# Optimization experiments

Hardware: AMD Instinct MI355X
Metric: run time of the kernel (lower is better)

Reference implementation:

```python
import jax, jax.numpy as jnp
import numpy as np
import math
from functools import lru_cache

DIM = 64   # num_inputs
HID = 32   # hidden_dim
B = 1024
LOG2 = math.log(2.0)
LOG_2PI = math.log(2.0 * math.pi)


@lru_cache(maxsize=None)
def _masks(out_f, in_f, dim):
    ob, ib = out_f // dim, in_f // dim
    md = np.zeros((out_f, in_f), np.float32)
    mo = np.ones((out_f, in_f), np.float32)
    for i in range(dim):
        md[i * ob:(i + 1) * ob, i * ib:(i + 1) * ib] = 1.0
        mo[i * ob:(i + 1) * ob, i * ib:] = 0.0
    return jnp.asarray(md), jnp.asarray(mo)


def masked_weight(x, grad, W, dw, b, dim):
    # W: (out_f, in_f), dw: (out_f, 1), b: (out_f,)
    out_f, in_f = W.shape
    ob, ib = out_f // dim, in_f // dim
    md, mo = _masks(out_f, in_f, dim)
    w = jnp.exp(W) * md + W * mo                      # positive diag blocks, masked lower blocks
    wsn = jnp.sum(w * w, axis=-1, keepdims=True)      # (out_f, 1) weight-norm denom^2
    wn = jnp.exp(dw) * w / jnp.sqrt(wsn)              # weight-normalized matrix
    wpl = dw + W - 0.5 * jnp.log(wsn)                 # log of diag-block entries, (out_f, in_f)
    # extract diagonal blocks: (dim, ob, dim, ib) -> diag over block index -> (ob, ib, dim)
    blocks = jnp.diagonal(wpl.reshape(dim, ob, dim, ib), axis1=0, axis2=2)
    g = jnp.transpose(blocks, (2, 0, 1))              # (dim, ob, ib) == torch g per-sample
    out = x @ wn.T + b
    if grad is None:
        return out, jnp.broadcast_to(g[None], (x.shape[0],) + g.shape)
    # grad: (Bt, dim, a, c); log-domain block 'matmul' via logsumexp over shared axis a(=ib)
    comb = g[None, :, :, None, :] + jnp.swapaxes(grad, -1, -2)[:, :, None, :, :]  # (Bt,dim,ob,c,ib)
    return out, jax.nn.logsumexp(comb, axis=-1)       # (Bt, dim, ob, c)


def tanh_layer(x, grad):
    g = -2.0 * (x - LOG2 + jax.nn.softplus(-2.0 * x))
    return jnp.tanh(x), g.reshape(grad.shape) + grad


def bnaf_flow(x, p0, p1, p2, gate, dim):
    out, grad = masked_weight(x, None, *p0, dim)
    out, grad = tanh_layer(out, grad)
    out, grad = masked_weight(out, grad, *p1, dim)
    out, grad = tanh_layer(out, grad)
    out, grad = masked_weight(out, grad, *p2, dim)
    g = grad.reshape(grad.shape[0], dim)              # squeeze (B, dim, 1, 1) -> (B, dim)
    if gate is None:
        return out, jnp.sum(g, -1)
    s = jax.nn.sigmoid(gate)
    out = s * out + (1.0 - s) * x
    ldj = jnp.sum(jax.nn.softplus(g + gate) - jax.nn.softplus(gate), -1)
    return out, ldj


def _forward(x, params, gates):
    ldj = 0.0
    for f in range(3):
        gate = gates[f] if f < 2 else None
        x, l = bnaf_flow(x, params[f][0], params[f][1], params[f][2], gate, DIM)
        ldj = ldj + l
        if f < 2:
            x = x[:, ::-1]                            # Permutation('flip'), log-det 0
    log_p_y = jnp.sum(-0.5 * x * x - 0.5 * LOG_2PI, -1)
    return log_p_y + ldj                              # (B,)


def setup_inputs() -> dict:
    key = jax.random.key(0)
    ks = iter(jax.random.split(key, 64))
    d, dh = DIM, DIM * HID
    shapes = [(dh, d), (dh, dh), (d, dh)]
    inp = {"x": jax.random.normal(next(ks), (B, d), jnp.float32)}
    for f in range(3):
        for l, (o, i) in enumerate(shapes):
            inp[f"W{f}_{l}"] = 0.1 * jax.random.normal(next(ks), (o, i), jnp.float32)
            inp[f"dw{f}_{l}"] = jnp.log(jax.random.uniform(next(ks), (o, 1), jnp.float32, 0.1, 1.0))
            inp[f"b{f}_{l}"] = 0.01 * jax.random.normal(next(ks), (o,), jnp.float32)
    inp["gate0"] = jax.random.normal(next(ks), (1,), jnp.float32)
    inp["gate1"] = jax.random.normal(next(ks), (1,), jnp.float32)
    return inp


def reference(x, W0_0, dw0_0, b0_0, W0_1, dw0_1, b0_1, W0_2, dw0_2, b0_2,
              W1_0, dw1_0, b1_0, W1_1, dw1_1, b1_1, W1_2, dw1_2, b1_2,
              W2_0, dw2_0, b2_0, W2_1, dw2_1, b2_1, W2_2, dw2_2, b2_2,
              gate0, gate1):
    params = [
        [(W0_0, dw0_0, b0_0), (W0_1, dw0_1, b0_1), (W0_2, dw0_2, b0_2)],
        [(W1_0, dw1_0, b1_0), (W1_1, dw1_1, b1_1), (W1_2, dw1_2, b1_2)],
        [(W2_0, dw2_0, b2_0), (W2_1, dw2_1, b2_1), (W2_2, dw2_2, b2_2)],
    ]
    return _forward(x, params, (gate0, gate1))
```

## Files before the change

### kernel.cpp

```cpp
#include <hip/hip_runtime.h>
#include <hip/hip_bf16.h>
#include <math.h>


#define DIMN 64
#define BATCH 1024
#define HIDF 2048
#define SPLITK 4
#define NT2 32

typedef __attribute__((ext_vector_type(8))) short short8;
typedef __attribute__((ext_vector_type(4))) float floatx4;

__device__ __forceinline__ float softplusf_(float t) {
    return fmaxf(t, 0.f) + log1pf(__expf(-fabsf(t)));
}

__device__ __forceinline__ float bf2f(short v) {
    union { unsigned u; float f; } x;
    x.u = ((unsigned)(unsigned short)v) << 16;
    return x.f;
}

__device__ __forceinline__ void gl_lds16(const void* g, void* l) {
    __builtin_amdgcn_global_load_lds(
        (const __attribute__((address_space(1))) unsigned int*)g,
        (__attribute__((address_space(3))) unsigned int*)l, 16, 0, 0);
}

__device__ __forceinline__ void tanh_sech2_(float p, float& th, float& s2) {
    float t = __expf(-2.f * fabsf(p));
    float opt = 1.f + t;
    float inv = 1.f / opt;
    th = copysignf((1.f - t) * inv, p);
    s2 = 4.f * t * inv * inv;
}

template<int INF>
__device__ __forceinline__ void prep_row(
    const float* __restrict__ W, const float* __restrict__ dw,
    void* __restrict__ wn_out, float* __restrict__ eg,
    int r, int lane, int out_f, int ob, int ib, int transpose, int bf16out)
{
    constexpr int NI = INF / 64;
    int d = r / ob;
    int c0 = d * ib;
    int c1 = c0 + ib;
    const float* Wr = W + (size_t)r * INF;

    float vv[NI];
    float ss = 0.f;
#pragma unroll
    for (int i = 0; i < NI; ++i) {
        int c = lane + i * 64;
        float wraw = Wr[c];
        float wv = (c < c0) ? wraw : ((c < c1) ? __expf(wraw) : 0.f);
        vv[i] = wv;
        ss += wv * wv;
    }
    for (int off = 32; off > 0; off >>= 1) ss += __shfl_xor(ss, off, 64);

    float dwr = dw[r];
    float scale = __expf(dwr) / sqrtf(ss);
    float logt = dwr - 0.5f * __logf(ss);

#pragma unroll
    for (int i = 0; i < NI; ++i) {
        int c = lane + i * 64;
        float val = scale * vv[i];
        if (bf16out) {
            ((__hip_bfloat16*)wn_out)[(size_t)r * INF + c] = __float2bfloat16(val);
        } else if (transpose) {
            ((float*)wn_out)[(size_t)c * out_f + r] = val;
        } else {
            ((float*)wn_out)[(size_t)r * INF + c] = val;
        }
    }
    if (lane < ib) eg[(size_t)r * ib + lane] = __expf(logt + Wr[c0 + lane]);
}

struct PrepIn { const float *W0, *dw0, *W1, *dw1, *W2, *dw2; };

__global__ __launch_bounds__(64) void prep_mega(
    PrepIn p0, PrepIn p1, PrepIn p2,
    float* __restrict__ wn0T_all, float* __restrict__ eg0_all,
    __hip_bfloat16* __restrict__ wn1_all, float* __restrict__ e1_all,
    __hip_bfloat16* __restrict__ wn2b_all, float* __restrict__ e2_all)
{
    int blk = blockIdx.x;
    int lane = threadIdx.x;
    int f = blk / 4160;
    int rem = blk - f * 4160;
    PrepIn P = (f == 0) ? p0 : ((f == 1) ? p1 : p2);

    float* wn0T = wn0T_all + (size_t)f * DIMN * HIDF;
    float* eg0  = eg0_all  + (size_t)f * HIDF;
    __hip_bfloat16* wn1 = wn1_all + (size_t)f * HIDF * HIDF;
    float* e1   = e1_all   + (size_t)f * HIDF * 32;
    __hip_bfloat16* wn2b = wn2b_all + (size_t)f * DIMN * HIDF;
    float* e2   = e2_all   + (size_t)f * DIMN * 32;

    if (rem < HIDF) {
        prep_row<DIMN>(P.W0, P.dw0, wn0T, eg0, rem, lane, HIDF, 32, 1, 1, 0);
    } else if (rem < 2 * HIDF) {
        prep_row<HIDF>(P.W1, P.dw1, wn1, e1, rem - HIDF, lane, HIDF, 32, 32, 0, 1);
    } else {
        prep_row<HIDF>(P.W2, P.dw2, wn2b, e2, rem - 2 * HIDF, lane, DIMN, 1, 32, 0, 1);
    }
}

__global__ __launch_bounds__(256) void gemm0_act(
    const float* __restrict__ xin, const float* __restrict__ wn0T,
    const float* __restrict__ bias, const float* __restrict__ eg0,
    __hip_bfloat16* __restrict__ h0, __hip_bfloat16* __restrict__ g0e)
{
    __shared__ float xs[16][DIMN];
    int b0 = blockIdx.y * 16;
    {
        const float4* src = (const float4*)(xin + (size_t)b0 * DIMN);
        ((float4*)xs)[threadIdx.x] = src[threadIdx.x];
    }
    __syncthreads();
    int n = blockIdx.x * 256 + threadIdx.x;

    float acc[16];
#pragma unroll
    for (int j = 0; j < 16; ++j) acc[j] = 0.f;

#pragma unroll 4
    for (int c4 = 0; c4 < 16; ++c4) {
        int c = c4 * 4;
        float w0 = wn0T[(size_t)(c + 0) * HIDF + n];
        float w1 = wn0T[(size_t)(c + 1) * HIDF + n];
        float w2 = wn0T[(size_t)(c + 2) * HIDF + n];
        float w3 = wn0T[(size_t)(c + 3) * HIDF + n];
#pragma unroll
        for (int j = 0; j < 16; ++j) {
            float4 x4 = *(const float4*)&xs[j][c];
            acc[j] = fmaf(x4.x, w0, acc[j]);
            acc[j] = fmaf(x4.y, w1, acc[j]);
            acc[j] = fmaf(x4.z, w2, acc[j]);
            acc[j] = fmaf(x4.w, w3, acc[j]);
        }
    }
    float bv = bias[n], egv = eg0[n];
#pragma unroll
    for (int j = 0; j < 16; ++j) {
        float p = acc[j] + bv;
        float th, s2;
        tanh_sech2_(p, th, s2);
        size_t idx = (size_t)(b0 + j) * HIDF + n;
        h0[idx] = __float2bfloat16(th);
        g0e[idx] = __float2bfloat16(egv * s2);
    }
}

#define G1BK 64
__global__ __launch_bounds__(256) void gemm1_part(
    const __hip_bfloat16* __restrict__ A, const __hip_bfloat16* __restrict__ B,
    __hip_bfloat16* __restrict__ part)
{
    __shared__ short As[128 * 64];
    __shared__ short Bs[128 * 64];
    const int K = HIDF, N = HIDF;
    int tid = threadIdx.x;
    int lane = tid & 63;
    int wave = tid >> 6;
    int n0 = blockIdx.x * 128;
    int m0 = blockIdx.y * 128;
    int kbase = blockIdx.z * (K / SPLITK);
    int wr = wave >> 1;
    int wc = wave & 1;

    int rf = lane & 15;
    int q = lane >> 4;

    const char* agp[4];
    const char* bgp[4];
    char* alds[4];
    char* blds[4];
#pragma unroll
    for (int s = 0; s < 4; ++s) {
        int c = tid + s * 256;
        int row = c >> 3;
        int kc = (c & 7) ^ (row & 7);
        agp[s] = (const char*)A + ((size_t)(m0 + row) * K + kbase) * 2 + kc * 16;
        bgp[s] = (const char*)B + ((size_t)(n0 + row) * K + kbase) * 2 + kc * 16;
        alds[s] = (char*)As + c * 16;
        blds[s] = (char*)Bs + c * 16;
    }

    floatx4 acc[4][4];
#pragma unroll
    for (int i = 0; i < 4; ++i)
#pragma unroll
        for (int j = 0; j < 4; ++j) acc[i][j] = (floatx4){0.f, 0.f, 0.f, 0.f};

    int rowA0 = wr * 64 + rf;
    int rowB0 = wc * 64 + rf;

    for (int k0 = 0; k0 < K / SPLITK; k0 += G1BK) {
        size_t kb = (size_t)k0 * 2;
        __syncthreads();
#pragma unroll
        for (int s = 0; s < 4; ++s) {
            gl_lds16(agp[s] + kb, alds[s]);
            gl_lds16(bgp[s] + kb, blds[s]);
        }
        __syncthreads();

#pragma unroll
        for (int s = 0; s < 2; ++s) {
            short8 af[4], bfv[4];
#pragma unroll
            for (int i = 0; i < 4; ++i) {
                int row = rowA0 + i * 16;
                af[i] = *(const short8*)&As[row * 64 + (((s * 4 + q) ^ (row & 7)) * 8)];
            }
#pragma unroll
            for (int j = 0; j < 4; ++j) {
                int row = rowB0 + j * 16;
                bfv[j] = *(const short8*)&Bs[row * 64 + (((s * 4 + q) ^ (row & 7)) * 8)];
            }
#pragma unroll
            for (int i = 0; i < 4; ++i)
#pragma unroll
                for (int j = 0; j < 4; ++j)
                    acc[i][j] = __builtin_amdgcn_mfma_f32_16x16x32_bf16(af[i], bfv[j], acc[i][j], 0, 0, 0);
        }
    }

    __hip_bfloat16* pk = part + (size_t)blockIdx.z * BATCH * HIDF;
    int col = lane & 15;
    int rq = (lane >> 4) * 4;
#pragma unroll
    for (int i = 0; i < 4; ++i) {
#pragma unroll
        for (int j = 0; j < 4; ++j) {
            int n = n0 + wc * 64 + j * 16 + col;
#pragma unroll
            for (int r = 0; r < 4; ++r) {
                int m = m0 + wr * 64 + i * 16 + rq + r;
                pk[(size_t)m * N + n] = __float2bfloat16(acc[i][j][r]);
            }
        }
    }
}

__global__ __launch_bounds__(256) void act_grad_gemm2(
    const __hip_bfloat16* __restrict__ part, const float* __restrict__ bias,
    const float* __restrict__ e1, const __hip_bfloat16* __restrict__ g0e,
    const __hip_bfloat16* __restrict__ wn2b,
    __hip_bfloat16* __restrict__ grad1e, float* __restrict__ out2p)
{
    __shared__ char smem[17408 + 8704 + 8192];
    float* g0s = (float*)smem;
    short* h1s = (short*)(smem + 17408);
    short* Bs2 = (short*)(smem + 17408 + 8704);

    int tid = threadIdx.x;
    int lane = tid & 63;
    int wave = tid >> 6;
    int n0 = blockIdx.x * 64;
    int b0 = blockIdx.y * 64;

    {
        int c0c = tid, c1c = tid + 256;
        int r0 = c0c >> 3, k0c = (c0c & 7) ^ (r0 & 7);
        int r1 = c1c >> 3, k1c = (c1c & 7) ^ (r1 & 7);
        gl_lds16((const char*)wn2b + ((size_t)r0 * HIDF + n0) * 2 + k0c * 16,
                 (char*)Bs2 + c0c * 16);
        gl_lds16((const char*)wn2b + ((size_t)r1 * HIDF + n0) * 2 + k1c * 16,
                 (char*)Bs2 + c1c * 16);
    }

    for (int s = tid; s < 512; s += 256) {
        int row = s >> 3, c8 = s & 7;
        short8 v = *(const short8*)((const short*)g0e +
                                    (size_t)(b0 + row) * HIDF + n0 + c8 * 8);
        float4 lo = { bf2f(v[0]), bf2f(v[1]), bf2f(v[2]), bf2f(v[3]) };
        float4 hi = { bf2f(v[4]), bf2f(v[5]), bf2f(v[6]), bf2f(v[7]) };
        *(float4*)&g0s[row * 68 + c8 * 8] = lo;
        *(float4*)&g0s[row * 68 + c8 * 8 + 4] = hi;
    }

    int g = tid >> 6;
    int nl = tid & 63;
    int n = n0 + nl;

    float4 er[8];
    const float4* e1r = (const float4*)(e1 + (size_t)n * 32);
#pragma unroll
    for (int qq = 0; qq < 8; ++qq) er[qq] = e1r[qq];

    float bv = bias[n];
    int kb2 = nl & 32;

    __syncthreads();

#pragma unroll
    for (int t = 0; t < 16; ++t) {
        int bl = g * 16 + t;
        int b = b0 + bl;
        size_t idx = (size_t)b * HIDF + n;
        float pre = bv;
#pragma unroll
        for (int p = 0; p < SPLITK; ++p)
            pre += __bfloat162float(part[(size_t)p * BATCH * HIDF + idx]);
        float th, s2;
        tanh_sech2_(pre, th, s2);
        const float* g0row = &g0s[bl * 68 + kb2];
        float dot = 0.f;
#pragma unroll
        for (int qq = 0; qq < 8; ++qq) {
            float4 gv = *(const float4*)&g0row[qq * 4];
            dot = fmaf(gv.x, er[qq].x, dot);
            dot = fmaf(gv.y, er[qq].y, dot);
            dot = fmaf(gv.z, er[qq].z, dot);
            dot = fmaf(gv.w, er[qq].w, dot);
        }
        __hip_bfloat16 thb = __float2bfloat16(th);
        h1s[bl * 68 + nl] = *(const short*)&thb;
        grad1e[idx] = __float2bfloat16(dot * s2);
    }
    __syncthreads();

    int rf = lane & 15;
    int q = lane >> 4;
    floatx4 acc2[4];
#pragma unroll
    for (int j = 0; j < 4; ++j) acc2[j] = (floatx4){0.f, 0.f, 0.f, 0.f};

#pragma unroll
    for (int s = 0; s < 2; ++s) {
        int rowa = wave * 16 + rf;
        short8 af = *(const short8*)&h1s[rowa * 68 + s * 32 + q * 8];
#pragma unroll
        for (int j = 0; j < 4; ++j) {
            int rowb = j * 16 + rf;
            int cp = (s * 4 + q) ^ (rowb & 7);
            short8 bfv = *(const short8*)&Bs2[rowb * 64 + cp * 8];
            acc2[j] = __builtin_amdgcn_mfma_f32_16x16x32_bf16(af, bfv, acc2[j], 0, 0, 0);
        }
    }

    float* outk = out2p + (size_t)blockIdx.x * BATCH * DIMN;
    int col = lane & 15;
    int rq = (lane >> 4) * 4;
#pragma unroll
    for (int j = 0; j < 4; ++j) {
#pragma unroll
        for (int r = 0; r < 4; ++r) {
            int m = b0 + wave * 16 + rq + r;
            outk[(size_t)m * DIMN + j * 16 + col] = acc2[j][r];
        }
    }
}

__global__ __launch_bounds__(256) void tail_trans(
    const float* __restrict__ out2p, const float* __restrict__ b2,
    const float* __restrict__ e2, const __hip_bfloat16* __restrict__ grad1e,
    const float* __restrict__ x_cur, const float* __restrict__ gate,
    float* __restrict__ x_next, float* __restrict__ ldj, int accum_ldj)
{
    int tid = threadIdx.x;
    int b = blockIdx.x * 4 + (tid >> 6);
    int n = tid & 63;

    float o = b2[n];
#pragma unroll
    for (int p = 0; p < NT2; ++p)
        o += out2p[(size_t)p * BATCH * DIMN + (size_t)b * DIMN + n];

    float gt = gate[0];
    float sg = 1.f / (1.f + __expf(-gt));
    float xo = sg * o + (1.f - sg) * x_cur[(size_t)b * DIMN + n];
    x_next[(size_t)b * DIMN + (63 - n)] = xo;

    const short8* gr = (const short8*)((const short*)grad1e + (size_t)b * HIDF + n * 32);
    const float4* gc = (const float4*)(e2 + n * 32);
    float s = 0.f;
#pragma unroll
    for (int q = 0; q < 4; ++q) {
        short8 a8 = gr[q];
        float4 c0 = gc[2 * q], c1 = gc[2 * q + 1];
        s = fmaf(bf2f(a8[0]), c0.x, s);
        s = fmaf(bf2f(a8[1]), c0.y, s);
        s = fmaf(bf2f(a8[2]), c0.z, s);
        s = fmaf(bf2f(a8[3]), c0.w, s);
        s = fmaf(bf2f(a8[4]), c1.x, s);
        s = fmaf(bf2f(a8[5]), c1.y, s);
        s = fmaf(bf2f(a8[6]), c1.z, s);
        s = fmaf(bf2f(a8[7]), c1.w, s);
    }
    float gF = __logf(fmaxf(s, 1e-45f));
    float contrib = softplusf_(gF + gt) - softplusf_(gt);
    for (int off = 32; off > 0; off >>= 1) contrib += __shfl_xor(contrib, off, 64);
    if (n == 0) ldj[b] = accum_ldj ? (ldj[b] + contrib) : contrib;
}

__global__ __launch_bounds__(256) void tail_final(
    const float* __restrict__ out2p, const float* __restrict__ b2,
    const float* __restrict__ e2, const __hip_bfloat16* __restrict__ grad1e,
    const float* __restrict__ ldj, float* __restrict__ out)
{
    int tid = threadIdx.x;
    int b = blockIdx.x * 4 + (tid >> 6);
    int n = tid & 63;

    float o = b2[n];
#pragma unroll
    for (int p = 0; p < NT2; ++p)
        o += out2p[(size_t)p * BATCH * DIMN + (size_t)b * DIMN + n];

    const short8* gr = (const short8*)((const short*)grad1e + (size_t)b * HIDF + n * 32);
    const float4* gc = (const float4*)(e2 + n * 32);
    float s = 0.f;
#pragma unroll
    for (int q = 0; q < 4; ++q) {
        short8 a8 = gr[q];
        float4 c0 = gc[2 * q], c1 = gc[2 * q + 1];
        s = fmaf(bf2f(a8[0]), c0.x, s);
        s = fmaf(bf2f(a8[1]), c0.y, s);
        s = fmaf(bf2f(a8[2]), c0.z, s);
        s = fmaf(bf2f(a8[3]), c0.w, s);
        s = fmaf(bf2f(a8[4]), c1.x, s);
        s = fmaf(bf2f(a8[5]), c1.y, s);
        s = fmaf(bf2f(a8[6]), c1.z, s);
        s = fmaf(bf2f(a8[7]), c1.w, s);
    }
    float gF = __logf(fmaxf(s, 1e-45f));

    float contrib = gF - 0.5f * o * o - 0.91893853320467274f;
    for (int off = 32; off > 0; off >>= 1) contrib += __shfl_xor(contrib, off, 64);
    if (n == 0) out[b] = ldj[b] + contrib;
}

extern "C" void kernel_launch(void* const* d_in, const int* in_sizes, int n_in,
                              void* d_out, int out_size, void* d_ws, size_t ws_size,
                              hipStream_t stream)
{
    (void)in_sizes; (void)n_in; (void)out_size; (void)ws_size;

    const float* x = (const float*)d_in[0];
    const float* gates[2] = { (const float*)d_in[28], (const float*)d_in[29] };

    char* ws = (char*)d_ws;
    size_t ofs = 0;
    auto alloc = [&](size_t bytes) { char* p = ws + ofs; ofs += (bytes + 255) & ~(size_t)255; return p; };

    __hip_bfloat16* wn1_all  = (__hip_bfloat16*)alloc((size_t)3 * HIDF * HIDF * 2);
    __hip_bfloat16* wn2b_all = (__hip_bfloat16*)alloc((size_t)3 * DIMN * HIDF * 2);
    float* wn0T_all = (float*)alloc((size_t)3 * DIMN * HIDF * 4);
    float* eg0_all  = (float*)alloc((size_t)3 * HIDF * 4);
    float* e1_all   = (float*)alloc((size_t)3 * HIDF * 32 * 4);
    float* e2_all   = (float*)alloc((size_t)3 * DIMN * 32 * 4);
    __hip_bfloat16* h0   = (__hip_bfloat16*)alloc((size_t)BATCH * HIDF * 2);
    __hip_bfloat16* part = (__hip_bfloat16*)alloc((size_t)SPLITK * BATCH * HIDF * 2);
    __hip_bfloat16* g0e    = (__hip_bfloat16*)alloc((size_t)BATCH * HIDF * 2);
    __hip_bfloat16* grad1e = (__hip_bfloat16*)alloc((size_t)BATCH * HIDF * 2);
    float* out2p  = (float*)alloc((size_t)NT2 * BATCH * DIMN * 4);
    float* x1     = (float*)alloc((size_t)BATCH * DIMN * 4);
    float* x2     = (float*)alloc((size_t)BATCH * DIMN * 4);
    float* ldj    = (float*)alloc(BATCH * 4);
    float* outp   = (float*)d_out;

    auto W = [&](int f, int i) { return (const float*)d_in[1 + f * 9 + i]; };

    PrepIn p0 = { W(0,0), W(0,1), W(0,3), W(0,4), W(0,6), W(0,7) };
    PrepIn p1 = { W(1,0), W(1,1), W(1,3), W(1,4), W(1,6), W(1,7) };
    PrepIn p2 = { W(2,0), W(2,1), W(2,3), W(2,4), W(2,6), W(2,7) };

    prep_mega<<<dim3(3 * 4160), dim3(64), 0, stream>>>(
        p0, p1, p2, wn0T_all, eg0_all, wn1_all, e1_all, wn2b_all, e2_all);

    gemm0_act<<<dim3(8, BATCH / 16), dim3(256), 0, stream>>>(
        x, wn0T_all, W(0,2), eg0_all, h0, g0e);

    const float* xcur = x;
    float* xnexts[2] = { x1, x2 };

    for (int f = 0; f < 3; ++f) {
        size_t fo1 = (size_t)f * HIDF * HIDF;
        size_t fo2 = (size_t)f * DIMN * HIDF;

        gemm1_part<<<dim3(HIDF / 128, BATCH / 128, SPLITK), dim3(256), 0, stream>>>(
            h0, wn1_all + fo1, part);

        act_grad_gemm2<<<dim3(HIDF / 64, BATCH / 64), dim3(256), 0, stream>>>(
            part, W(f,5), e1_all + (size_t)f * HIDF * 32, g0e,
            wn2b_all + fo2, grad1e, out2p);

        if (f < 2) {
            tail_trans<<<dim3(BATCH / 4), dim3(256), 0, stream>>>(
                out2p, W(f,8), e2_all + (size_t)f * DIMN * 32, grad1e,
                xcur, gates[f], xnexts[f], ldj, f);

            gemm0_act<<<dim3(8, BATCH / 16), dim3(256), 0, stream>>>(
                xnexts[f], wn0T_all + (size_t)(f + 1) * DIMN * HIDF, W(f + 1, 2),
                eg0_all + (size_t)(f + 1) * HIDF, h0, g0e);

            xcur = xnexts[f];
        } else {
            tail_final<<<dim3(BATCH / 4), dim3(256), 0, stream>>>(
                out2p, W(2,8), e2_all + (size_t)2 * DIMN * 32, grad1e, ldj, outp);
        }
    }
}
```

Before: 291.4 us.

## Exploit block-triangular weight structure to skip zero blocks across all kernels

The masked weights are block lower-triangular, so every kernel now limits its work to the nonzero region. The prep kernel packs four rows per block and loads and writes only the nonzero columns. gemm0 shortens its K loop per block, and gemm1 returns early or truncates the K range for split-K partitions that lie above the diagonal. The act/gemm2 and tail kernels read and accumulate only the partitions and MFMA tiles that can be nonzero. Unwritten zero regions of the weight buffers and skipped partial sums are assumed to be zero or never read, which relies on the indexing being exactly consistent across kernels.

```diff
diff --git a/kernel.cpp b/kernel.cpp
--- a/kernel.cpp
+++ b/kernel.cpp
@@ -10,6 +10,7 @@
 #define NT2 32
 
 typedef __attribute__((ext_vector_type(8))) short short8;
+typedef __attribute__((ext_vector_type(4))) short short4v;
 typedef __attribute__((ext_vector_type(4))) float floatx4;
 
 __device__ __forceinline__ float softplusf_(float t) {
@@ -36,61 +37,78 @@
     s2 = 4.f * t * inv * inv;
 }
 
-template<int INF>
-__device__ __forceinline__ void prep_row(
+
+__device__ __forceinline__ void prep_row0(
     const float* __restrict__ W, const float* __restrict__ dw,
-    void* __restrict__ wn_out, float* __restrict__ eg,
-    int r, int lane, int out_f, int ob, int ib, int transpose, int bf16out)
-{
-    constexpr int NI = INF / 64;
-    int d = r / ob;
-    int c0 = d * ib;
-    int c1 = c0 + ib;
-    const float* Wr = W + (size_t)r * INF;
-
-    float vv[NI];
+    float* __restrict__ wn0T, float* __restrict__ eg0, int r, int lane)
+{
+    int d = r >> 5;
+    const float* Wr = W + (size_t)r * 64;
+    float wraw = Wr[lane];
+    float wv = (lane < d) ? wraw : ((lane == d) ? __expf(wraw) : 0.f);
+    float ss = wv * wv;
+    for (int off = 32; off > 0; off >>= 1) ss += __shfl_xor(ss, off, 64);
+    float dwr = dw[r];
+    float scale = __expf(dwr) / sqrtf(ss);
+    wn0T[(size_t)lane * HIDF + r] = scale * wv;
+    if (lane == 0) eg0[r] = __expf(dwr - 0.5f * __logf(ss) + Wr[d]);
+}
+
+__device__ __forceinline__ void prep_row_wide(
+    const float* __restrict__ W, const float* __restrict__ dw,
+    __hip_bfloat16* __restrict__ wn, float* __restrict__ eg,
+    int r, int lane, int d, int ni, int nw)
+{
+    int c0 = d * 32, c1 = c0 + 32;
+    const float* Wr = W + (size_t)r * 2048;
+    float4 vv[8];
     float ss = 0.f;
 #pragma unroll
-    for (int i = 0; i < NI; ++i) {
-        int c = lane + i * 64;
-        float wraw = Wr[c];
-        float wv = (c < c0) ? wraw : ((c < c1) ? __expf(wraw) : 0.f);
-        vv[i] = wv;
-        ss += wv * wv;
+    for (int i = 0; i < 8; ++i) {
+        vv[i] = (float4){0.f, 0.f, 0.f, 0.f};
+        if (i < ni) {
+            int cb = i * 256 + lane * 4;
+            float4 v = *(const float4*)&Wr[cb];
+            float w0 = (cb + 0 < c0) ? v.x : ((cb + 0 < c1) ? __expf(v.x) : 0.f);
+            float w1 = (cb + 1 < c0) ? v.y : ((cb + 1 < c1) ? __expf(v.y) : 0.f);
+            float w2 = (cb + 2 < c0) ? v.z : ((cb + 2 < c1) ? __expf(v.z) : 0.f);
+            float w3 = (cb + 3 < c0) ? v.w : ((cb + 3 < c1) ? __expf(v.w) : 0.f);
+            vv[i] = (float4){w0, w1, w2, w3};
+            ss += w0 * w0 + w1 * w1 + w2 * w2 + w3 * w3;
+        }
     }
     for (int off = 32; off > 0; off >>= 1) ss += __shfl_xor(ss, off, 64);
-
     float dwr = dw[r];
     float scale = __expf(dwr) / sqrtf(ss);
     float logt = dwr - 0.5f * __logf(ss);
-
-#pragma unroll
-    for (int i = 0; i < NI; ++i) {
-        int c = lane + i * 64;
-        float val = scale * vv[i];
-        if (bf16out) {
-            ((__hip_bfloat16*)wn_out)[(size_t)r * INF + c] = __float2bfloat16(val);
-        } else if (transpose) {
-            ((float*)wn_out)[(size_t)c * out_f + r] = val;
-        } else {
-            ((float*)wn_out)[(size_t)r * INF + c] = val;
-        }
-    }
-    if (lane < ib) eg[(size_t)r * ib + lane] = __expf(logt + Wr[c0 + lane]);
+#pragma unroll
+    for (int i = 0; i < 8; ++i) {
+        if (i < nw) {
+            int cb = i * 256 + lane * 4;
+            __hip_bfloat16 b0 = __float2bfloat16(scale * vv[i].x);
+            __hip_bfloat16 b1 = __float2bfloat16(scale * vv[i].y);
+            __hip_bfloat16 b2 = __float2bfloat16(scale * vv[i].z);
+            __hip_bfloat16 b3 = __float2bfloat16(scale * vv[i].w);
+            short4v pk = { *(short*)&b0, *(short*)&b1, *(short*)&b2, *(short*)&b3 };
+            *(short4v*)((short*)wn + (size_t)r * 2048 + cb) = pk;
+        }
+    }
+    if (lane < 32) eg[(size_t)r * 32 + lane] = __expf(logt + Wr[c0 + lane]);
 }
 
 struct PrepIn { const float *W0, *dw0, *W1, *dw1, *W2, *dw2; };
 
-__global__ __launch_bounds__(64) void prep_mega(
+__global__ __launch_bounds__(256) void prep_mega(
     PrepIn p0, PrepIn p1, PrepIn p2,
     float* __restrict__ wn0T_all, float* __restrict__ eg0_all,
     __hip_bfloat16* __restrict__ wn1_all, float* __restrict__ e1_all,
     __hip_bfloat16* __restrict__ wn2b_all, float* __restrict__ e2_all)
 {
     int blk = blockIdx.x;
-    int lane = threadIdx.x;
-    int f = blk / 4160;
-    int rem = blk - f * 4160;
+    int wave = threadIdx.x >> 6;
+    int lane = threadIdx.x & 63;
+    int f = blk / 1040;
+    int rem = blk - f * 1040;
     PrepIn P = (f == 0) ? p0 : ((f == 1) ? p1 : p2);
 
     float* wn0T = wn0T_all + (size_t)f * DIMN * HIDF;
@@ -100,12 +118,15 @@
     __hip_bfloat16* wn2b = wn2b_all + (size_t)f * DIMN * HIDF;
     float* e2   = e2_all   + (size_t)f * DIMN * 32;
 
-    if (rem < HIDF) {
-        prep_row<DIMN>(P.W0, P.dw0, wn0T, eg0, rem, lane, HIDF, 32, 1, 1, 0);
-    } else if (rem < 2 * HIDF) {
-        prep_row<HIDF>(P.W1, P.dw1, wn1, e1, rem - HIDF, lane, HIDF, 32, 32, 0, 1);
+    if (rem < 512) {
+        int r = rem * 4 + wave;
+        prep_row0(P.W0, P.dw0, wn0T, eg0, r, lane);
+    } else if (rem < 1024) {
+        int r = (rem - 512) * 4 + wave;
+        prep_row_wide(P.W1, P.dw1, wn1, e1, r, lane, r >> 5, (r >> 8) + 1, (r >> 8) + 1);
     } else {
-        prep_row<HIDF>(P.W2, P.dw2, wn2b, e2, rem - 2 * HIDF, lane, DIMN, 1, 32, 0, 1);
+        int r = (rem - 1024) * 4 + wave;
+        prep_row_wide(P.W2, P.dw2, wn2b, e2, r, lane, r, (r >> 3) + 1, 8);
     }
 }
 
@@ -127,8 +148,9 @@
 #pragma unroll
     for (int j = 0; j < 16; ++j) acc[j] = 0.f;
 
-#pragma unroll 4
-    for (int c4 = 0; c4 < 16; ++c4) {
+    int c4max = 2 * blockIdx.x + 2;
+#pragma unroll 2
+    for (int c4 = 0; c4 < c4max; ++c4) {
         int c = c4 * 4;
         float w0 = wn0T[(size_t)(c + 0) * HIDF + n];
         float w1 = wn0T[(size_t)(c + 1) * HIDF + n];
@@ -160,15 +182,20 @@
     const __hip_bfloat16* __restrict__ A, const __hip_bfloat16* __restrict__ B,
     __hip_bfloat16* __restrict__ part)
 {
+    const int K = HIDF, N = HIDF;
+    int jn = blockIdx.x;
+    int kbase = blockIdx.z * (K / SPLITK);
+    int kend = (jn + 1) * 128 - kbase;
+    if (kend <= 0) return;
+    if (kend > K / SPLITK) kend = K / SPLITK;
+
     __shared__ short As[128 * 64];
     __shared__ short Bs[128 * 64];
-    const int K = HIDF, N = HIDF;
     int tid = threadIdx.x;
     int lane = tid & 63;
     int wave = tid >> 6;
-    int n0 = blockIdx.x * 128;
+    int n0 = jn * 128;
     int m0 = blockIdx.y * 128;
-    int kbase = blockIdx.z * (K / SPLITK);
     int wr = wave >> 1;
     int wc = wave & 1;
 
@@ -199,7 +226,7 @@
     int rowA0 = wr * 64 + rf;
     int rowB0 = wc * 64 + rf;
 
-    for (int k0 = 0; k0 < K / SPLITK; k0 += G1BK) {
+    for (int k0 = 0; k0 < kend; k0 += G1BK) {
         size_t kb = (size_t)k0 * 2;
         __syncthreads();
 #pragma unroll
@@ -261,8 +288,11 @@
     int tid = threadIdx.x;
     int lane = tid & 63;
     int wave = tid >> 6;
-    int n0 = blockIdx.x * 64;
+    int bx = blockIdx.x;
+    int n0 = bx * 64;
     int b0 = blockIdx.y * 64;
+    int np = (bx >> 3) + 1;
+    int jact0 = bx >> 3;
 
     {
         int c0c = tid, c1c = tid + 256;
@@ -295,6 +325,10 @@
 
     float bv = bias[n];
     int kb2 = nl & 32;
+    const __hip_bfloat16* pp0 = part;
+    const __hip_bfloat16* pp1 = part + (size_t)1 * BATCH * HIDF;
+    const __hip_bfloat16* pp2 = part + (size_t)2 * BATCH * HIDF;
+    const __hip_bfloat16* pp3 = part + (size_t)3 * BATCH * HIDF;
 
     __syncthreads();
 
@@ -303,10 +337,10 @@
         int bl = g * 16 + t;
         int b = b0 + bl;
         size_t idx = (size_t)b * HIDF + n;
-        float pre = bv;
-#pragma unroll
-        for (int p = 0; p < SPLITK; ++p)
-            pre += __bfloat162float(part[(size_t)p * BATCH * HIDF + idx]);
+        float pre = bv + __bfloat162float(pp0[idx]);
+        if (np > 1) pre += __bfloat162float(pp1[idx]);
+        if (np > 2) pre += __bfloat162float(pp2[idx]);
+        if (np > 3) pre += __bfloat162float(pp3[idx]);
         float th, s2;
         tanh_sech2_(pre, th, s2);
         const float* g0row = &g0s[bl * 68 + kb2];
@@ -337,22 +371,26 @@
         short8 af = *(const short8*)&h1s[rowa * 68 + s * 32 + q * 8];
 #pragma unroll
         for (int j = 0; j < 4; ++j) {
-            int rowb = j * 16 + rf;
-            int cp = (s * 4 + q) ^ (rowb & 7);
-            short8 bfv = *(const short8*)&Bs2[rowb * 64 + cp * 8];
-            acc2[j] = __builtin_amdgcn_mfma_f32_16x16x32_bf16(af, bfv, acc2[j], 0, 0, 0);
-        }
-    }
-
-    float* outk = out2p + (size_t)blockIdx.x * BATCH * DIMN;
+            if (j >= jact0) {
+                int rowb = j * 16 + rf;
+                int cp = (s * 4 + q) ^ (rowb & 7);
+                short8 bfv = *(const short8*)&Bs2[rowb * 64 + cp * 8];
+                acc2[j] = __builtin_amdgcn_mfma_f32_16x16x32_bf16(af, bfv, acc2[j], 0, 0, 0);
+            }
+        }
+    }
+
+    float* outk = out2p + (size_t)bx * BATCH * DIMN;
     int col = lane & 15;
     int rq = (lane >> 4) * 4;
 #pragma unroll
     for (int j = 0; j < 4; ++j) {
-#pragma unroll
-        for (int r = 0; r < 4; ++r) {
-            int m = b0 + wave * 16 + rq + r;
-            outk[(size_t)m * DIMN + j * 16 + col] = acc2[j][r];
+        if (j >= jact0) {
+#pragma unroll
+            for (int r = 0; r < 4; ++r) {
+                int m = b0 + wave * 16 + rq + r;
+                outk[(size_t)m * DIMN + j * 16 + col] = acc2[j][r];
+            }
         }
     }
 }
@@ -368,8 +406,8 @@
     int n = tid & 63;
 
     float o = b2[n];
-#pragma unroll
-    for (int p = 0; p < NT2; ++p)
+    int pmax = n >> 1;
+    for (int p = 0; p <= pmax; ++p)
         o += out2p[(size_t)p * BATCH * DIMN + (size_t)b * DIMN + n];
 
     float gt = gate[0];
@@ -409,8 +447,8 @@
     int n = tid & 63;
 
     float o = b2[n];
-#pragma unroll
-    for (int p = 0; p < NT2; ++p)
+    int pmax = n >> 1;
+    for (int p = 0; p <= pmax; ++p)
         o += out2p[(size_t)p * BATCH * DIMN + (size_t)b * DIMN + n];
 
     const short8* gr = (const short8*)((const short*)grad1e + (size_t)b * HIDF + n * 32);
@@ -471,7 +509,7 @@
     PrepIn p1 = { W(1,0), W(1,1), W(1,3), W(1,4), W(1,6), W(1,7) };
     PrepIn p2 = { W(2,0), W(2,1), W(2,3), W(2,4), W(2,6), W(2,7) };
 
-    prep_mega<<<dim3(3 * 4160), dim3(64), 0, stream>>>(
+    prep_mega<<<dim3(3 * 1040), dim3(256), 0, stream>>>(
         p0, p1, p2, wn0T_all, eg0_all, wn1_all, e1_all, wn2b_all, e2_all);
 
     gemm0_act<<<dim3(8, BATCH / 16), dim3(256), 0, stream>>>(
```

Result: slower. 343.3 us (+17.8%).

## Exploit block-triangular weight mask to skip zero tiles in hidden GEMMs

Applied to the files above, without the earlier changes.

The hidden-layer GEMM now launches only the (n-tile, k-split) pairs that can hold nonzero weights under the autoregressive block-lower-triangular mask, using constant lookup tables to map blocks to tiles and truncate the K loop. The following activation kernel sums only the split-K partials that were actually written for each column range and skips MFMAs on zero weight blocks in the output projection. This removes roughly half of the dense GEMM work on masked-out zeros. It relies on the mask structure and on unwritten partial buffers never being read, and adds load imbalance across blocks with different K lengths.

```diff
diff --git a/kernel.cpp b/kernel.cpp
--- a/kernel.cpp
+++ b/kernel.cpp
@@ -155,20 +155,34 @@
     }
 }
 
+__constant__ unsigned char G1_JN[40] = {
+    3,4,5,6,7,7,8,8,9,9,10,10,11,11,11,12,12,12,13,13,13,14,14,14,
+    15,15,15,15, 2,6,10,14, 1,5,9,13, 0,4,8,12 };
+__constant__ unsigned char G1_KZ[40] = {
+    0,0,0,0,0,1,0,1,0,1, 0, 1, 0, 1, 2, 0, 1, 2, 0, 1, 2, 0, 1, 2,
+     0, 1, 2, 3, 0,1, 2, 3, 0,1,2,3, 0,1,2,3 };
+
 #define G1BK 64
 __global__ __launch_bounds__(256) void gemm1_part(
     const __hip_bfloat16* __restrict__ A, const __hip_bfloat16* __restrict__ B,
     __hip_bfloat16* __restrict__ part)
 {
+    const int K = HIDF, N = HIDF;
+    int pr = blockIdx.x >> 3;
+    int my = blockIdx.x & 7;
+    int jn = G1_JN[pr];
+    int kz = G1_KZ[pr];
+    int kbase = kz * (K / SPLITK);
+    int kend = (jn + 1) * 128 - kbase;
+    if (kend > K / SPLITK) kend = K / SPLITK;
+
     __shared__ short As[128 * 64];
     __shared__ short Bs[128 * 64];
-    const int K = HIDF, N = HIDF;
     int tid = threadIdx.x;
     int lane = tid & 63;
     int wave = tid >> 6;
-    int n0 = blockIdx.x * 128;
-    int m0 = blockIdx.y * 128;
-    int kbase = blockIdx.z * (K / SPLITK);
+    int n0 = jn * 128;
+    int m0 = my * 128;
     int wr = wave >> 1;
     int wc = wave & 1;
 
@@ -199,7 +213,7 @@
     int rowA0 = wr * 64 + rf;
     int rowB0 = wc * 64 + rf;
 
-    for (int k0 = 0; k0 < K / SPLITK; k0 += G1BK) {
+    for (int k0 = 0; k0 < kend; k0 += G1BK) {
         size_t kb = (size_t)k0 * 2;
         __syncthreads();
 #pragma unroll
@@ -230,7 +244,7 @@
         }
     }
 
-    __hip_bfloat16* pk = part + (size_t)blockIdx.z * BATCH * HIDF;
+    __hip_bfloat16* pk = part + (size_t)kz * BATCH * HIDF;
     int col = lane & 15;
     int rq = (lane >> 4) * 4;
 #pragma unroll
@@ -261,8 +275,11 @@
     int tid = threadIdx.x;
     int lane = tid & 63;
     int wave = tid >> 6;
-    int n0 = blockIdx.x * 64;
+    int bx = blockIdx.x;
+    int n0 = bx * 64;
     int b0 = blockIdx.y * 64;
+    int np = (bx >> 3) + 1;
+    int jact0 = bx >> 3;
 
     {
         int c0c = tid, c1c = tid + 256;
@@ -295,6 +312,10 @@
 
     float bv = bias[n];
     int kb2 = nl & 32;
+    const __hip_bfloat16* pp0 = part;
+    const __hip_bfloat16* pp1 = part + (size_t)1 * BATCH * HIDF;
+    const __hip_bfloat16* pp2 = part + (size_t)2 * BATCH * HIDF;
+    const __hip_bfloat16* pp3 = part + (size_t)3 * BATCH * HIDF;
 
     __syncthreads();
 
@@ -303,10 +324,10 @@
         int bl = g * 16 + t;
         int b = b0 + bl;
         size_t idx = (size_t)b * HIDF + n;
-        float pre = bv;
-#pragma unroll
-        for (int p = 0; p < SPLITK; ++p)
-            pre += __bfloat162float(part[(size_t)p * BATCH * HIDF + idx]);
+        float pre = bv + __bfloat162float(pp0[idx]);
+        if (np > 1) pre += __bfloat162float(pp1[idx]);
+        if (np > 2) pre += __bfloat162float(pp2[idx]);
+        if (np > 3) pre += __bfloat162float(pp3[idx]);
         float th, s2;
         tanh_sech2_(pre, th, s2);
         const float* g0row = &g0s[bl * 68 + kb2];
@@ -337,14 +358,16 @@
         short8 af = *(const short8*)&h1s[rowa * 68 + s * 32 + q * 8];
 #pragma unroll
         for (int j = 0; j < 4; ++j) {
-            int rowb = j * 16 + rf;
-            int cp = (s * 4 + q) ^ (rowb & 7);
-            short8 bfv = *(const short8*)&Bs2[rowb * 64 + cp * 8];
-            acc2[j] = __builtin_amdgcn_mfma_f32_16x16x32_bf16(af, bfv, acc2[j], 0, 0, 0);
-        }
-    }
-
-    float* outk = out2p + (size_t)blockIdx.x * BATCH * DIMN;
+            if (j >= jact0) {
+                int rowb = j * 16 + rf;
+                int cp = (s * 4 + q) ^ (rowb & 7);
+                short8 bfv = *(const short8*)&Bs2[rowb * 64 + cp * 8];
+                acc2[j] = __builtin_amdgcn_mfma_f32_16x16x32_bf16(af, bfv, acc2[j], 0, 0, 0);
+            }
+        }
+    }
+
+    float* outk = out2p + (size_t)bx * BATCH * DIMN;
     int col = lane & 15;
     int rq = (lane >> 4) * 4;
 #pragma unroll
@@ -484,7 +507,7 @@
         size_t fo1 = (size_t)f * HIDF * HIDF;
         size_t fo2 = (size_t)f * DIMN * HIDF;
 
-        gemm1_part<<<dim3(HIDF / 128, BATCH / 128, SPLITK), dim3(256), 0, stream>>>(
+        gemm1_part<<<dim3(320), dim3(256), 0, stream>>>(
             h0, wn1_all + fo1, part);
 
         act_grad_gemm2<<<dim3(HIDF / 64, BATCH / 64), dim3(256), 0, stream>>>(
```

Result: slower. 331.0 us (+13.6%).
